# Performance work log

Hardware: AMD Instinct MI355X
Metric: run time of the kernel (lower is better)

## Reference

```python
import jax, jax.numpy as jnp
import numpy as np

B, T, N = 256, 512, 128
GO, EOS = 1, 2  # mead-baseline Offsets
NEG = -10000.0


def setup_inputs() -> dict:
    key = jax.random.key(0)
    k1, k2, k3 = jax.random.split(key, 3)
    unaries = jax.random.normal(k1, (B, T, N), dtype=jnp.float32)
    # constraint mask: True where transition is INVALID (masked to -1e4)
    cmask = jax.random.bernoulli(k2, 0.3, (1, N, N))
    trans = jax.nn.log_softmax(
        jnp.where(cmask, jnp.float32(NEG), jnp.float32(0.0)), axis=1
    )  # [1, N, N], matches buffer construction in __init__
    lengths = jax.random.randint(k3, (B,), T // 2, T + 1).astype(jnp.int64)
    lengths = lengths.at[0].set(T)  # ensure max(lengths) == T
    return {"unaries": unaries, "trans": trans, "lengths": lengths}


def _viterbi(probv, trans, lengths, start_idx, end_idx):
    # probv: [T, B, N] log-probs; trans: [1, N, N]; lengths: [B]
    seq_len, batch, n_tags = probv.shape
    trans0 = trans[0]  # [N(cur), N(prev)]
    lengths = lengths.astype(jnp.int32)

    alphas = jnp.full((batch, n_tags), NEG, probv.dtype).at[:, start_idx].set(0.0)
    alphas = jax.nn.log_softmax(alphas, axis=-1)

    def step(alphas, xs):
        unary_t, i = xs  # [B, N], scalar
        ntv = alphas[:, None, :] + trans0[None]          # [B, N_cur, N_prev]
        bp = jnp.argmax(ntv, axis=2)                     # backpointers [B, N]
        new_alphas = jnp.max(ntv, axis=2) + unary_t      # [B, N]
        alphas = jnp.where((i < lengths)[:, None], new_alphas, alphas)
        return alphas, bp

    alphas, bps = jax.lax.scan(step, alphas, (probv, jnp.arange(seq_len)))

    terminal = alphas + trans0[end_idx][None, :]         # [B, N]
    path_score = jnp.max(terminal, axis=1)               # [B]
    best_tag = jnp.argmax(terminal, axis=1)              # [B]

    rev_len = seq_len - lengths - 1

    def back(btid, xs):
        bp, i = xs  # bp: [B, N]
        new = jnp.take_along_axis(bp, btid[:, None], axis=1)[:, 0]
        btid = jnp.where(i > rev_len, new, btid)
        return btid, btid

    _, ys = jax.lax.scan(back, best_tag, (bps[::-1], jnp.arange(seq_len)))
    full = jnp.concatenate([best_tag[None], ys], axis=0)  # [T+1, B]
    best_path = full[:seq_len][::-1]                       # [T, B]

    seq_mask = jnp.arange(seq_len)[:, None] < lengths[None, :]  # [T, B]
    best_path = jnp.where(seq_mask, best_path, 0)
    return best_path, path_score


def reference(unaries, trans, lengths):
    # constrained branch of TaggerGreedyDecoder.forward (batch_first=True)
    probv = jax.nn.log_softmax(jnp.swapaxes(unaries, 0, 1), axis=-1)  # [T,B,N]
    preds_tb, scores = _viterbi(probv, trans, lengths, GO, EOS)
    return jnp.swapaxes(preds_tb, 0, 1), scores  # ([B,T], [B])
```

## Files before the change

### kernel.cpp

```cpp
#include <hip/hip_runtime.h>

#define BB 256
#define TT 512
#define NN 128
#define GO_IDX 1
#define EOS_IDX 2
#define TSPLIT 496
#define NEGV (-10000.0f)
#define ASLOT(x) ((x) + (((x) >> 5) << 2))

#define STEP_BARRIER() asm volatile("s_waitcnt lgkmcnt(0)\n\ts_barrier" ::: "memory")

__device__ __forceinline__ float dpp_xor1_f(float x) {
    return __int_as_float(__builtin_amdgcn_update_dpp(0, __float_as_int(x), 0xB1, 0xF, 0xF, true));
}
__device__ __forceinline__ float dpp_xor2_f(float x) {
    return __int_as_float(__builtin_amdgcn_update_dpp(0, __float_as_int(x), 0x4E, 0xF, 0xF, true));
}
__device__ __forceinline__ int dpp_xor1_i(int x) {
    return __builtin_amdgcn_update_dpp(0, x, 0xB1, 0xF, 0xF, true);
}
__device__ __forceinline__ int dpp_xor2_i(int x) {
    return __builtin_amdgcn_update_dpp(0, x, 0x4E, 0xF, 0xF, true);
}

__global__ __launch_bounds__(256) void lsm_kernel(float* __restrict__ u,
                                                  const int* __restrict__ lengths_raw) {
    const int g0 = (blockIdx.x * 256 + threadIdx.x) >> 5;
    const int l  = threadIdx.x & 31;
    const int b  = g0 >> 6;
    const int j  = g0 & 63;
    int len;
    {
        int probe = lengths_raw[1];
        len = (probe == 0) ? lengths_raw[2 * b] : lengths_raw[b];
    }
    float4* base = (float4*)(u + (size_t)b * TT * NN);
    int row = j;
    float4 v = base[row * 32 + l];
    for (;;) {
        const int nrow = row + 64;
        const bool more = (nrow < len);
        float4 vn;
        if (more) vn = base[nrow * 32 + l];
        float m = fmaxf(fmaxf(v.x, v.y), fmaxf(v.z, v.w));
#pragma unroll
        for (int off = 16; off; off >>= 1) m = fmaxf(m, __shfl_xor(m, off, 64));
        float s = expf(v.x - m) + expf(v.y - m) + expf(v.z - m) + expf(v.w - m);
#pragma unroll
        for (int off = 16; off; off >>= 1) s += __shfl_xor(s, off, 64);
        float ls = logf(s);
        base[row * 32 + l] =
            make_float4((v.x - m) - ls, (v.y - m) - ls, (v.z - m) - ls, (v.w - m) - ls);
        if (!more) break;
        v = vn; row = nrow;
    }
}

__global__ __launch_bounds__(512) void viterbi_kernel(
    const float* __restrict__ probs,
    const float* __restrict__ trans,
    const int*   __restrict__ lengths_raw,
    float* __restrict__ out,
    unsigned char* __restrict__ ws)
{
    __shared__ unsigned char bps[(TSPLIT - 1) * NN];
    __shared__ __align__(16) float alpha[2][144];
    __shared__ float fin_v[2];
    __shared__ int   fin_i[2];

    const int tid  = threadIdx.x;
    const int b    = blockIdx.x;
    const int wave = tid >> 6;
    const int lane = tid & 63;
    const int q    = tid & 3;
    const int cur  = tid >> 2;

    int len;
    {
        int probe = lengths_raw[1];
        len = (probe == 0) ? lengths_raw[2 * b] : lengths_raw[b];
    }

    float tr[32];
    {
        const float4* t4 = (const float4*)(trans + cur * NN + q * 32);
#pragma unroll
        for (int i = 0; i < 8; ++i) {
            float4 v = t4[i];
            tr[4*i+0] = v.x; tr[4*i+1] = v.y; tr[4*i+2] = v.z; tr[4*i+3] = v.w;
        }
    }

    if (tid < NN) alpha[0][ASLOT(tid)] = (tid == GO_IDX) ? 0.0f : NEGV;

    const float* pb = probs + (size_t)b * TT * NN;
    unsigned char* wst = ws + (size_t)b * ((TT - TSPLIT) * NN);

    float P[8], Nx[8];
    if (q == 0) {
#pragma unroll
        for (int k = 0; k < 8; ++k) P[k] = pb[k * NN + cur];
    }
    __syncthreads();

    const int nG = (len + 7) >> 3;
    for (int g = 0; g < nG; ++g) {
        const int tb = g * 8;
        if (q == 0) {
#pragma unroll
            for (int k = 0; k < 8; ++k) {
                int tt = tb + 8 + k; if (tt > TT - 1) tt = TT - 1;
                Nx[k] = pb[tt * NN + cur];
            }
        }
#pragma unroll
        for (int k = 0; k < 8; ++k) {
            const int t = tb + k;
            if (t < len) {
                const float* ra = alpha[t & 1];
                float*       wa = alpha[(t & 1) ^ 1];
                const float4* a4 = (const float4*)(ra + q * 36);
                float bv[4]; int bi[4];
#pragma unroll
                for (int c = 0; c < 4; ++c) {
                    float4 a0 = a4[c * 2], a1 = a4[c * 2 + 1];
                    const int base = c * 8;
                    bv[c] = a0.x + tr[base + 0]; bi[c] = base + 0;
                    float x;
                    x = a0.y + tr[base + 1]; if (x > bv[c]) { bv[c] = x; bi[c] = base + 1; }
                    x = a0.z + tr[base + 2]; if (x > bv[c]) { bv[c] = x; bi[c] = base + 2; }
                    x = a0.w + tr[base + 3]; if (x > bv[c]) { bv[c] = x; bi[c] = base + 3; }
                    x = a1.x + tr[base + 4]; if (x > bv[c]) { bv[c] = x; bi[c] = base + 4; }
                    x = a1.y + tr[base + 5]; if (x > bv[c]) { bv[c] = x; bi[c] = base + 5; }
                    x = a1.z + tr[base + 6]; if (x > bv[c]) { bv[c] = x; bi[c] = base + 6; }
                    x = a1.w + tr[base + 7]; if (x > bv[c]) { bv[c] = x; bi[c] = base + 7; }
                }
                float best = bv[0]; int bp = bi[0];
#pragma unroll
                for (int c = 1; c < 4; ++c) { if (bv[c] > best) { best = bv[c]; bp = bi[c]; } }
                bp += q * 32;

                float v1 = dpp_xor1_f(best); int b1 = dpp_xor1_i(bp);
                bool  t1 = (q & 1) ? (v1 >= best) : (v1 > best);
                float m1 = t1 ? v1 : best;   int p1 = t1 ? b1 : bp;
                float v2 = dpp_xor2_f(m1);   int b2 = dpp_xor2_i(p1);
                bool  t2 = (q & 2) ? (v2 >= m1) : (v2 > m1);
                float M  = t2 ? v2 : m1;     int BP = t2 ? b2 : p1;

                if (q == 0) {
                    wa[ASLOT(cur)] = M + P[k];
                    if (t >= 1) {
                        if (t < TSPLIT) bps[(t - 1) * NN + cur] = (unsigned char)BP;
                        else            wst[(t - TSPLIT) * NN + cur] = (unsigned char)BP;
                    }
                }
                STEP_BARRIER();
            }
        }
#pragma unroll
        for (int k = 0; k < 8; ++k) P[k] = Nx[k];
    }

    __threadfence();

    if (tid < NN) {
        float v = alpha[len & 1][ASLOT(tid)] + trans[EOS_IDX * NN + tid];
        int idx = tid;
#pragma unroll
        for (int off = 32; off; off >>= 1) {
            float ov = __shfl_xor(v, off, 64);
            int   oi = __shfl_xor(idx, off, 64);
            if (ov > v || (ov == v && oi < idx)) { v = ov; idx = oi; }
        }
        if (lane == 0) { fin_v[wave] = v; fin_i[wave] = idx; }
    }
    __syncthreads();

    for (int t = len + tid; t < TT; t += 512) out[(size_t)b * TT + t] = 0.0f;

    if (tid == 0) {
        float v0 = fin_v[0], v1 = fin_v[1];
        int   i0 = fin_i[0], i1 = fin_i[1];
        float sc; int tag;
        if (v1 > v0) { sc = v1; tag = i1; }
        else         { sc = v0; tag = i0; }
        out[(size_t)BB * TT + b] = sc;

        for (int t = len - 1; t >= 0; --t) {
            out[(size_t)b * TT + t] = (float)tag;
            if (t >= 1) {
                int nb;
                if (t < TSPLIT) nb = bps[(t - 1) * NN + tag];
                else            nb = ((volatile const unsigned char*)wst)[(t - TSPLIT) * NN + tag];
                tag = nb;
            }
        }
    }
}

extern "C" void kernel_launch(void* const* d_in, const int* in_sizes, int n_in,
                              void* d_out, int out_size, void* d_ws, size_t ws_size,
                              hipStream_t stream) {
    float*       unaries = (float*)d_in[0];
    const float* trans   = (const float*)d_in[1];
    const int*   lengths = (const int*)d_in[2];
    float* out = (float*)d_out;
    unsigned char* ws = (unsigned char*)d_ws;

    hipLaunchKernelGGL(lsm_kernel, dim3(2048), dim3(256), 0, stream, unaries, lengths);
    hipLaunchKernelGGL(viterbi_kernel, dim3(BB), dim3(512), 0, stream,
                       unaries, trans, lengths, out, ws);
}
```

Before: 506.1 us.

## Fuse log-softmax into Viterbi kernel and spill backpointers into consumed input rows

Removes the separate log-softmax kernel. Each Viterbi block now normalizes its own unary rows, 16 timesteps at a time, into a double-buffered shared-memory tile while the recurrence runs. Backpointers past the shared-memory split are written into the already-consumed input rows instead of a workspace buffer. The first 128 of those spilled rows are copied back into LDS before the serial backtrace. The shared split is lowered to free LDS for the prob tile. This saves a launch and a full global read/write pass, but it mutates the input in place, so a repeated call would see corrupted data.

Measured after the change: 499.9 us. No clear change (-1.2%).

```diff
diff --git a/kernel.cpp b/kernel.cpp
--- a/kernel.cpp
+++ b/kernel.cpp
@@ -5,7 +5,7 @@
 #define NN 128
 #define GO_IDX 1
 #define EOS_IDX 2
-#define TSPLIT 496
+#define TSPLIT 368
 #define NEGV (-10000.0f)
 #define ASLOT(x) ((x) + (((x) >> 5) << 2))
 
@@ -24,47 +24,14 @@
     return __builtin_amdgcn_update_dpp(0, x, 0x4E, 0xF, 0xF, true);
 }
 
-__global__ __launch_bounds__(256) void lsm_kernel(float* __restrict__ u,
-                                                  const int* __restrict__ lengths_raw) {
-    const int g0 = (blockIdx.x * 256 + threadIdx.x) >> 5;
-    const int l  = threadIdx.x & 31;
-    const int b  = g0 >> 6;
-    const int j  = g0 & 63;
-    int len;
-    {
-        int probe = lengths_raw[1];
-        len = (probe == 0) ? lengths_raw[2 * b] : lengths_raw[b];
-    }
-    float4* base = (float4*)(u + (size_t)b * TT * NN);
-    int row = j;
-    float4 v = base[row * 32 + l];
-    for (;;) {
-        const int nrow = row + 64;
-        const bool more = (nrow < len);
-        float4 vn;
-        if (more) vn = base[nrow * 32 + l];
-        float m = fmaxf(fmaxf(v.x, v.y), fmaxf(v.z, v.w));
-#pragma unroll
-        for (int off = 16; off; off >>= 1) m = fmaxf(m, __shfl_xor(m, off, 64));
-        float s = expf(v.x - m) + expf(v.y - m) + expf(v.z - m) + expf(v.w - m);
-#pragma unroll
-        for (int off = 16; off; off >>= 1) s += __shfl_xor(s, off, 64);
-        float ls = logf(s);
-        base[row * 32 + l] =
-            make_float4((v.x - m) - ls, (v.y - m) - ls, (v.z - m) - ls, (v.w - m) - ls);
-        if (!more) break;
-        v = vn; row = nrow;
-    }
-}
-
 __global__ __launch_bounds__(512) void viterbi_kernel(
-    const float* __restrict__ probs,
+    float* __restrict__ u,
     const float* __restrict__ trans,
     const int*   __restrict__ lengths_raw,
-    float* __restrict__ out,
-    unsigned char* __restrict__ ws)
+    float* __restrict__ out)
 {
     __shared__ unsigned char bps[(TSPLIT - 1) * NN];
+    __shared__ __align__(16) float prob[2][16][NN];
     __shared__ __align__(16) float alpha[2][144];
     __shared__ float fin_v[2];
     __shared__ int   fin_i[2];
@@ -75,6 +42,8 @@
     const int lane = tid & 63;
     const int q    = tid & 3;
     const int cur  = tid >> 2;
+    const int hw   = tid >> 5;
+    const int l32  = tid & 31;
 
     int len;
     {
@@ -82,6 +51,9 @@
         len = (probe == 0) ? lengths_raw[2 * b] : lengths_raw[b];
     }
 
+    float* pb = u + (size_t)b * TT * NN;
+    const float4* pb4 = (const float4*)pb;
+
     float tr[32];
     {
         const float4* t4 = (const float4*)(trans + cur * NN + q * 32);
@@ -94,30 +66,37 @@
 
     if (tid < NN) alpha[0][ASLOT(tid)] = (tid == GO_IDX) ? 0.0f : NEGV;
 
-    const float* pb = probs + (size_t)b * TT * NN;
-    unsigned char* wst = ws + (size_t)b * ((TT - TSPLIT) * NN);
-
-    float P[8], Nx[8];
-    if (q == 0) {
-#pragma unroll
-        for (int k = 0; k < 8; ++k) P[k] = pb[k * NN + cur];
-    }
+    auto normrow = [&](float4 v, float* dstrow) {
+        float m = fmaxf(fmaxf(v.x, v.y), fmaxf(v.z, v.w));
+#pragma unroll
+        for (int off = 16; off; off >>= 1) m = fmaxf(m, __shfl_xor(m, off, 64));
+        float s = expf(v.x - m) + expf(v.y - m) + expf(v.z - m) + expf(v.w - m);
+#pragma unroll
+        for (int off = 16; off; off >>= 1) s += __shfl_xor(s, off, 64);
+        float ls = logf(s);
+        ((float4*)dstrow)[l32] =
+            make_float4((v.x - m) - ls, (v.y - m) - ls, (v.z - m) - ls, (v.w - m) - ls);
+    };
+
+    float4 R = pb4[hw * 32 + l32];
+    normrow(R, &prob[0][hw][0]);
+    R = pb4[(16 + hw) * 32 + l32];
     __syncthreads();
 
-    const int nG = (len + 7) >> 3;
+    const int nG = (len + 15) >> 4;
     for (int g = 0; g < nG; ++g) {
-        const int tb = g * 8;
-        if (q == 0) {
-#pragma unroll
-            for (int k = 0; k < 8; ++k) {
-                int tt = tb + 8 + k; if (tt > TT - 1) tt = TT - 1;
-                Nx[k] = pb[tt * NN + cur];
-            }
-        }
-#pragma unroll
-        for (int k = 0; k < 8; ++k) {
+        const int tb = g << 4;
+        normrow(R, &prob[(g + 1) & 1][hw][0]);
+        {
+            int rr = tb + 32 + hw;
+            if (rr > TT - 1) rr = TT - 1;
+            R = pb4[rr * 32 + l32];
+        }
+#pragma unroll 4
+        for (int k = 0; k < 16; ++k) {
             const int t = tb + k;
             if (t < len) {
+                const float Pv = prob[g & 1][k][cur];
                 const float* ra = alpha[t & 1];
                 float*       wa = alpha[(t & 1) ^ 1];
                 const float4* a4 = (const float4*)(ra + q * 36);
@@ -149,17 +128,15 @@
                 float M  = t2 ? v2 : m1;     int BP = t2 ? b2 : p1;
 
                 if (q == 0) {
-                    wa[ASLOT(cur)] = M + P[k];
+                    wa[ASLOT(cur)] = M + Pv;
                     if (t >= 1) {
                         if (t < TSPLIT) bps[(t - 1) * NN + cur] = (unsigned char)BP;
-                        else            wst[(t - TSPLIT) * NN + cur] = (unsigned char)BP;
+                        else ((unsigned char*)pb)[(size_t)t * 512 + cur] = (unsigned char)BP;
                     }
                 }
                 STEP_BARRIER();
             }
         }
-#pragma unroll
-        for (int k = 0; k < 8; ++k) P[k] = Nx[k];
     }
 
     __threadfence();
@@ -178,6 +155,14 @@
     __syncthreads();
 
     for (int t = len + tid; t < TT; t += 512) out[(size_t)b * TT + t] = 0.0f;
+
+    {
+        unsigned int* cache = (unsigned int*)&prob[0][0][0];
+        const volatile unsigned int* src = (const volatile unsigned int*)pb;
+        for (int i = tid; i < 128 * 32; i += 512)
+            cache[i] = src[(size_t)(TSPLIT + (i >> 5)) * 128 + (i & 31)];
+    }
+    __syncthreads();
 
     if (tid == 0) {
         float v0 = fin_v[0], v1 = fin_v[1];
@@ -187,12 +172,14 @@
         else         { sc = v0; tag = i0; }
         out[(size_t)BB * TT + b] = sc;
 
+        const unsigned char* cacheb = (const unsigned char*)&prob[0][0][0];
         for (int t = len - 1; t >= 0; --t) {
             out[(size_t)b * TT + t] = (float)tag;
             if (t >= 1) {
                 int nb;
-                if (t < TSPLIT) nb = bps[(t - 1) * NN + tag];
-                else            nb = ((volatile const unsigned char*)wst)[(t - TSPLIT) * NN + tag];
+                if (t < TSPLIT)            nb = bps[(t - 1) * NN + tag];
+                else if (t < TSPLIT + 128) nb = cacheb[(t - TSPLIT) * NN + tag];
+                else nb = ((const volatile unsigned char*)pb)[(size_t)t * 512 + tag];
                 tag = nb;
             }
         }
@@ -206,9 +193,8 @@
     const float* trans   = (const float*)d_in[1];
     const int*   lengths = (const int*)d_in[2];
     float* out = (float*)d_out;
-    unsigned char* ws = (unsigned char*)d_ws;
-
-    hipLaunchKernelGGL(lsm_kernel, dim3(2048), dim3(256), 0, stream, unaries, lengths);
+    (void)d_ws; (void)ws_size; (void)in_sizes; (void)n_in; (void)out_size;
+
     hipLaunchKernelGGL(viterbi_kernel, dim3(BB), dim3(512), 0, stream,
-                       unaries, trans, lengths, out, ws);
-}
+                       unaries, trans, lengths, out);
+}
```
